# Performance work log

Measured on AMD Instinct MI355X. Metric: run time of the kernel, lower is better.

Reference implementation:

```python
import jax, jax.numpy as jnp
import numpy as np

NUM_HEADS = 16

def setup_inputs() -> dict:
    key = jax.random.key(0)
    ks = jax.random.split(key, 7)
    B, Q, K, D = 4, 512, 4096, 1024
    return {
        'query':  jax.random.normal(ks[0], (B, Q, D), dtype=jnp.float32),
        'memory': jax.random.normal(ks[1], (B, K, D), dtype=jnp.float32),
        'bias':   jax.random.normal(ks[2], (B, K), dtype=jnp.float32),
        'Wq': jax.random.normal(ks[3], (D, D), dtype=jnp.float32) * (D ** -0.5),
        'Wk': jax.random.normal(ks[4], (D, D), dtype=jnp.float32) * (D ** -0.5),
        'Wv': jax.random.normal(ks[5], (D, D), dtype=jnp.float32) * (D ** -0.5),
        'Wo': jax.random.normal(ks[6], (D, D), dtype=jnp.float32) * (D ** -0.5),
    }

def reference(query, memory, bias, Wq, Wk, Wv, Wo):
    B, Qn, _ = query.shape
    _, Kn, _ = memory.shape
    H = NUM_HEADS
    E = Wq.shape[1]
    dh = E // H
    scale = dh ** -0.5
    # projections (bias-free linears), split heads: [B, H, len, dh]
    q = (query @ Wq).reshape(B, Qn, H, dh).transpose(0, 2, 1, 3)
    k = (memory @ Wk).reshape(B, Kn, H, dh).transpose(0, 2, 1, 3)
    v = (memory @ Wv).reshape(B, Kn, H, dh).transpose(0, 2, 1, 3)
    scores = jnp.einsum('bhqd,bhkd->bhqk', q, k) * scale
    scores = scores + bias[:, None, None, :]          # additive support bias over K
    weights = jax.nn.softmax(scores, axis=-1)          # dropout p=0.0 -> identity
    out = jnp.einsum('bhqk,bhkd->bhqd', weights, v)
    out = out.transpose(0, 2, 1, 3).reshape(B, Qn, E)
    return out @ Wo
```

## Files before the change

kernel.cpp:

```cpp
#include <hip/hip_runtime.h>

typedef __attribute__((ext_vector_type(8))) short bf16x8;
typedef __attribute__((ext_vector_type(4))) short bf16x4;
typedef __attribute__((ext_vector_type(4))) float f32x4;

#define MFMA32(a,b,c) __builtin_amdgcn_mfma_f32_16x16x32_bf16((a),(b),(c),0,0,0)
#define MFMA16(a,b,c) __builtin_amdgcn_mfma_f32_16x16x16bf16_1k((a),(b),(c),0,0,0)
#define LOG2E 1.44269504f

__device__ __forceinline__ unsigned short f2bf(float f) {
  unsigned int u = __float_as_uint(f);
  u += 0x7fffu + ((u >> 16) & 1u);
  return (unsigned short)(u >> 16);
}

__device__ __forceinline__ void cp16(const void* g, void* l) {
  __builtin_amdgcn_global_load_lds((const __attribute__((address_space(1))) void*)g,
                                   (__attribute__((address_space(3))) void*)l, 16, 0, 0);
}

__global__ void conv_both(const float* __restrict__ q, const float* __restrict__ m,
                          const float* __restrict__ bias,
                          unsigned short* __restrict__ qo, unsigned short* __restrict__ mo,
                          float* __restrict__ bz) {
  int i = blockIdx.x * 256 + threadIdx.x;
  if (i < 524288) {
    float4 v = ((const float4*)q)[i];
    ushort4 o; o.x = f2bf(v.x); o.y = f2bf(v.y); o.z = f2bf(v.z); o.w = f2bf(v.w);
    ((ushort4*)qo)[i] = o;
  } else if (i < 4718592) {
    int j = i - 524288;
    float4 v = ((const float4*)m)[j];
    ushort4 o; o.x = f2bf(v.x); o.y = f2bf(v.y); o.z = f2bf(v.z); o.w = f2bf(v.w);
    ((ushort4*)mo)[j] = o;
  } else {
    int j = i - 4718592;
    float4 v = ((const float4*)bias)[j];
    float4 o;
    o.x = __builtin_fmaf(v.x, LOG2E, -16.f);
    o.y = __builtin_fmaf(v.y, LOG2E, -16.f);
    o.z = __builtin_fmaf(v.z, LOG2E, -16.f);
    o.w = __builtin_fmaf(v.w, LOG2E, -16.f);
    ((float4*)bz)[j] = o;
  }
}

__global__ void transpose4(const float* __restrict__ Wq, const float* __restrict__ Wk,
                           const float* __restrict__ Wv, const float* __restrict__ Wo,
                           unsigned short* __restrict__ dst) {
  __shared__ float t[32][33];
  int z = blockIdx.z;
  const float* W = (z == 0) ? Wq : (z == 1) ? Wk : (z == 2) ? Wv : Wo;
  unsigned short* WT = dst + (size_t)z * 1048576;
  int bx = blockIdx.x * 32, by = blockIdx.y * 32;
  int x = threadIdx.x, y0 = threadIdx.y;
#pragma unroll
  for (int r = 0; r < 4; ++r)
    t[y0 + r * 8][x] = W[(size_t)(by + y0 + r * 8) * 1024 + bx + x];
  __syncthreads();
#pragma unroll
  for (int r = 0; r < 4; ++r)
    WT[(size_t)(bx + y0 + r * 8) * 1024 + by + x] = f2bf(t[x][y0 + r * 8]);
}

__global__ __launch_bounds__(256, 2) void gemm_kv(
    const unsigned short* __restrict__ A,
    const unsigned short* __restrict__ Bk,
    const unsigned short* __restrict__ Bv,
    unsigned short* __restrict__ Kp,
    unsigned short* __restrict__ Vt)
{
  __shared__ __attribute__((aligned(16))) unsigned short lds[32768];
  const int tid = threadIdx.x;
  const int w = tid >> 6, lane = tid & 63;
  const int lh = lane & 15, q4 = lane >> 4;
  const int id = blockIdx.x;
  const int xcd = id & 7, j = id >> 3;
  const int tm = (xcd * 16 + (j >> 4)) * 128;
  const int tn = (j & 15) * 64;
  const int wm = (w >> 1) * 64, wn = (w & 1) * 32;

  const int r8 = lane >> 3;
  const int scol = ((lane & 7) ^ r8) * 8;
  const int srow = w * 8 + r8;
  const int fs0 = ((0 + q4) ^ (lh & 7)) * 8;
  const int fs1 = ((4 + q4) ^ (lh & 7)) * 8;

  const unsigned short* Ag = A  + (size_t)tm * 1024 + scol;
  const unsigned short* Kg = Bk + (size_t)tn * 1024 + scol;
  const unsigned short* Vg = Bv + (size_t)tn * 1024 + scol;

#define STG(BUF,KT) do {                                                      \
    cp16(Ag + (size_t)( 0 + srow) * 1024 + (KT)*64, lds + (BUF)*16384 +         w*512); \
    cp16(Ag + (size_t)(32 + srow) * 1024 + (KT)*64, lds + (BUF)*16384 +  2048 + w*512); \
    cp16(Ag + (size_t)(64 + srow) * 1024 + (KT)*64, lds + (BUF)*16384 +  4096 + w*512); \
    cp16(Ag + (size_t)(96 + srow) * 1024 + (KT)*64, lds + (BUF)*16384 +  6144 + w*512); \
    cp16(Kg + (size_t)( 0 + srow) * 1024 + (KT)*64, lds + (BUF)*16384 +  8192 + w*512); \
    cp16(Kg + (size_t)(32 + srow) * 1024 + (KT)*64, lds + (BUF)*16384 + 10240 + w*512); \
    cp16(Vg + (size_t)( 0 + srow) * 1024 + (KT)*64, lds + (BUF)*16384 + 12288 + w*512); \
    cp16(Vg + (size_t)(32 + srow) * 1024 + (KT)*64, lds + (BUF)*16384 + 14336 + w*512); \
  } while (0)

  f32x4 acck[4][2] = {}, accv[4][2] = {};

  STG(0, 0);

  for (int t = 0; t < 16; ++t) {
    const unsigned short* bse = lds + (t & 1) * 16384;
    __syncthreads();
    if (t < 15) STG((t & 1) ^ 1, t + 1);
    {
      bf16x8 a0[4], bk0[2], bv0[2];
#pragma unroll
      for (int m = 0; m < 4; ++m)
        a0[m] = *(const bf16x8*)(bse + (wm + m * 16 + lh) * 64 + fs0);
#pragma unroll
      for (int n = 0; n < 2; ++n) {
        bk0[n] = *(const bf16x8*)(bse +  8192 + (wn + n * 16 + lh) * 64 + fs0);
        bv0[n] = *(const bf16x8*)(bse + 12288 + (wn + n * 16 + lh) * 64 + fs0);
      }
      __builtin_amdgcn_s_setprio(1);
#pragma unroll
      for (int m = 0; m < 4; ++m)
#pragma unroll
        for (int n = 0; n < 2; ++n) {
          acck[m][n] = MFMA32(a0[m], bk0[n], acck[m][n]);
          accv[m][n] = MFMA32(a0[m], bv0[n], accv[m][n]);
        }
      __builtin_amdgcn_s_setprio(0);
    }
    {
      bf16x8 a1[4], bk1[2], bv1[2];
#pragma unroll
      for (int m = 0; m < 4; ++m)
        a1[m] = *(const bf16x8*)(bse + (wm + m * 16 + lh) * 64 + fs1);
#pragma unroll
      for (int n = 0; n < 2; ++n) {
        bk1[n] = *(const bf16x8*)(bse +  8192 + (wn + n * 16 + lh) * 64 + fs1);
        bv1[n] = *(const bf16x8*)(bse + 12288 + (wn + n * 16 + lh) * 64 + fs1);
      }
      __builtin_amdgcn_s_setprio(1);
#pragma unroll
      for (int m = 0; m < 4; ++m)
#pragma unroll
        for (int n = 0; n < 2; ++n) {
          acck[m][n] = MFMA32(a1[m], bk1[n], acck[m][n]);
          accv[m][n] = MFMA32(a1[m], bv1[n], accv[m][n]);
        }
      __builtin_amdgcn_s_setprio(0);
    }
  }
#undef STG

#pragma unroll
  for (int m = 0; m < 4; ++m)
#pragma unroll
    for (int n = 0; n < 2; ++n) {
      int row = tm + wm + m * 16 + q4 * 4;
      int col = tn + wn + n * 16 + lh;
#pragma unroll
      for (int e = 0; e < 4; ++e)
        Kp[(size_t)(row + e) * 1024 + col] = f2bf(acck[m][n][e]);
    }

  __syncthreads();
#pragma unroll
  for (int m = 0; m < 4; ++m)
#pragma unroll
    for (int n = 0; n < 2; ++n) {
      int row = wm + m * 16 + q4 * 4;
      int col = wn + n * 16 + lh;
      ushort4 v4;
      v4.x = f2bf(accv[m][n][0]); v4.y = f2bf(accv[m][n][1]);
      v4.z = f2bf(accv[m][n][2]); v4.w = f2bf(accv[m][n][3]);
      *(ushort4*)(lds + col * 128 + (row ^ ((col & 15) << 3))) = v4;
    }
  __syncthreads();
#pragma unroll
  for (int p = 0; p < 4; ++p) {
    int col = p * 16 + (tid >> 4);
    int jb = tid & 15;
    const unsigned short* src = lds + col * 128 + ((jb ^ (col & 15)) << 3);
    *(int4*)(Vt + (size_t)(tn + col) * 16384 + tm + jb * 8) = *(const int4*)src;
  }
}

__global__ __launch_bounds__(256) void gemm_bt64(
    const unsigned short* __restrict__ A, const unsigned short* __restrict__ B,
    float* __restrict__ Cf, unsigned short* __restrict__ Cb,
    int M, int N, int K, float scale)
{
  __shared__ __attribute__((aligned(16))) unsigned short lds[24576];
  int w = threadIdx.x >> 6, lane = threadIdx.x & 63;
  int lh = lane & 15, q4 = lane >> 4;
  int tm = blockIdx.y * 128, tn = blockIdx.x * 64;
  int wm = (w & 1) * 64, wn = (w >> 1) * 32;

  int srow = lane >> 2;
  int scol = ((lane & 3) ^ ((lane >> 3) & 3)) << 3;
  int q4s = (q4 ^ ((lh >> 1) & 3)) << 3;

#define STG64(BUF,K0)                                                          \
  {                                                                            \
    _Pragma("unroll") for (int i = 0; i < 2; ++i) {                            \
      int c = w * 2 + i;                                                       \
      cp16(A + (size_t)(tm + c * 16 + srow) * K + (K0) + scol,                 \
           lds + (BUF) * 6144 + c * 512);                                      \
    }                                                                          \
    cp16(B + (size_t)(tn + w * 16 + srow) * K + (K0) + scol,                   \
         lds + (BUF) * 6144 + 4096 + w * 512);                                 \
  }

  f32x4 acc[4][2] = {};
  const int nw = K >> 6;

  STG64(0, 0);
  STG64(1, 32);

  for (int s = 0; s < nw; ++s) {
    __syncthreads();
    if (s + 1 < nw) {
      STG64((2 * s + 2) & 3, (2 * s + 2) << 5);
      STG64((2 * s + 3) & 3, (2 * s + 3) << 5);
    }
#pragma unroll
    for (int u = 0; u < 2; ++u) {
      const unsigned short* bse = lds + ((2 * s + u) & 3) * 6144;
      bf16x8 afr[4], bfr[2];
#pragma unroll
      for (int r = 0; r < 4; ++r)
        afr[r] = *(const bf16x8*)(bse + (wm + r * 16 + lh) * 32 + q4s);
#pragma unroll
      for (int c = 0; c < 2; ++c)
        bfr[c] = *(const bf16x8*)(bse + 4096 + (wn + c * 16 + lh) * 32 + q4s);
      __builtin_amdgcn_s_setprio(1);
#pragma unroll
      for (int r = 0; r < 4; ++r)
#pragma unroll
        for (int c = 0; c < 2; ++c)
          acc[r][c] = MFMA32(afr[r], bfr[c], acc[r][c]);
      __builtin_amdgcn_s_setprio(0);
    }
  }
#undef STG64

#pragma unroll
  for (int r = 0; r < 4; ++r)
#pragma unroll
    for (int c = 0; c < 2; ++c)
#pragma unroll
      for (int e = 0; e < 4; ++e) {
        int row = tm + wm + r * 16 + q4 * 4 + e;
        int col = tn + wn + c * 16 + lh;
        if (Cb) Cb[(size_t)row * N + col] = f2bf(acc[r][c][e] * scale);
        else    Cf[(size_t)row * N + col] = acc[r][c][e] * scale;
      }
}

__global__ __launch_bounds__(256) void attn_kernel(
    const unsigned short* __restrict__ Q, const unsigned short* __restrict__ Kp,
    const unsigned short* __restrict__ VT, const float* __restrict__ bz,
    float* __restrict__ po, float* __restrict__ lp)
{
  __shared__ __attribute__((aligned(16))) unsigned short Klds[8192];
  __shared__ __attribute__((aligned(16))) unsigned short Vlds[8192];
  int w = threadIdx.x >> 6, lane = threadIdx.x & 63;
  int lh = lane & 15, q4 = lane >> 4;

  int id = blockIdx.x;
  int xcd = id & 7, j = id >> 3;
  int ql = j & 7;
  int half = ql & 1, qt = ql >> 1;
  int bh = (j >> 3) * 8 + xcd;
  int b = bh >> 4, h = bh & 15;
  int q0 = qt * 128;
  int t00 = half * 2048;

  const unsigned short* Qb = Q + (size_t)(b * 512 + q0 + w * 32) * 1024 + h * 64;
  const unsigned short* Kb = Kp + (size_t)(b * 4096) * 1024 + h * 64;
  const unsigned short* Vb = VT + (size_t)(h * 64) * 16384 + b * 4096;
  const float* bzg = bz + (size_t)b * 4096;

  bf16x8 bq[2][2];
#pragma unroll
  for (int s = 0; s < 2; ++s)
#pragma unroll
    for (int th = 0; th < 2; ++th)
      bq[s][th] = *(const bf16x8*)(Qb + (size_t)(s * 16 + lh) * 1024 + th * 32 + q4 * 8);

  f32x4 oa[2][4] = {};
  float ls[2] = {0.f, 0.f};

  int rl = lane >> 3, blk = lane & 7;
  int sw = ((blk ^ rl) * 8);

  {
    int t = t00;
#pragma unroll
    for (int r = 0; r < 2; ++r) {
      int seg = r * 4 + w;
      int row = seg * 8 + rl;
      cp16(Kb + (size_t)(t + row) * 1024 + sw, Klds + seg * 512);
      cp16(Vb + (size_t)row * 16384 + t + sw, Vlds + seg * 512);
    }
  }

  for (int ti = 0; ti < 32; ++ti) {
    int t = t00 + ti * 64;
    __syncthreads();
    if (ti < 31) {
      int t2 = t + 64;
      int bo2 = ((ti + 1) & 1) * 4096;
#pragma unroll
      for (int r = 0; r < 2; ++r) {
        int seg = r * 4 + w;
        int row = seg * 8 + rl;
        cp16(Kb + (size_t)(t2 + row) * 1024 + sw, Klds + bo2 + seg * 512);
        cp16(Vb + (size_t)row * 16384 + t2 + sw, Vlds + bo2 + seg * 512);
      }
    }
    const unsigned short* Kl = Klds + (ti & 1) * 4096;
    const unsigned short* Vl = Vlds + (ti & 1) * 4096;

    float4 bz4[4];
#pragma unroll
    for (int c = 0; c < 4; ++c)
      bz4[c] = *(const float4*)(bzg + t + c * 16 + q4 * 4);

    bf16x8 kf[4][2];
#pragma unroll
    for (int c = 0; c < 4; ++c)
#pragma unroll
      for (int th = 0; th < 2; ++th)
        kf[c][th] = *(const bf16x8*)(Kl + (c * 16 + lh) * 64 + (((th << 2) + q4) ^ (lh & 7)) * 8);
    bf16x4 vf[4][4];
#pragma unroll
    for (int c = 0; c < 4; ++c)
#pragma unroll
      for (int c2 = 0; c2 < 4; ++c2)
        vf[c][c2] = *(const bf16x4*)(Vl + (c2 * 16 + lh) * 64 +
                                     (((c << 1) + (q4 >> 1)) ^ (lh & 7)) * 8 + (q4 & 1) * 4);

#pragma unroll
    for (int s = 0; s < 2; ++s) {
#pragma unroll
      for (int c = 0; c < 4; ++c) {
        f32x4 z = {};
        z = MFMA32(kf[c][0], bq[s][0], z);
        z = MFMA32(kf[c][1], bq[s][1], z);
        float bzf[4] = {bz4[c].x, bz4[c].y, bz4[c].z, bz4[c].w};
        bf16x4 pb;
        float ps = 0.f;
#pragma unroll
        for (int e = 0; e < 4; ++e) {
          float p = __builtin_amdgcn_exp2f(z[e] + bzf[e]);
          ps += p;
          pb[e] = (short)f2bf(p);
        }
        ls[s] += ps;
#pragma unroll
        for (int c2 = 0; c2 < 4; ++c2)
          oa[s][c2] = MFMA16(vf[c][c2], pb, oa[s][c2]);
      }
    }
  }

#pragma unroll
  for (int s = 0; s < 2; ++s) {
    ls[s] += __shfl_xor(ls[s], 16);
    ls[s] += __shfl_xor(ls[s], 32);
  }

  int sl = bh * 4 + qt;
  float* pslice = po + (size_t)(half * 256 + sl) * 8192;
#pragma unroll
  for (int s = 0; s < 2; ++s) {
    if (q4 == 0) lp[half * 32768 + sl * 128 + w * 32 + s * 16 + lh] = ls[s];
#pragma unroll
    for (int c2 = 0; c2 < 4; ++c2)
#pragma unroll
      for (int e = 0; e < 4; ++e)
        pslice[(c2 * 16 + q4 * 4 + e) * 128 + w * 32 + s * 16 + lh] = oa[s][c2][e];
  }
}

__global__ void norm_kernel(const float* __restrict__ po, const float* __restrict__ lp,
                            unsigned short* __restrict__ ao) {
  int g = blockIdx.x * 256 + threadIdx.x;
  int d8 = (g & 7) * 8;
  int rowid = g >> 3;
  int bh = rowid >> 9, rq = rowid & 511, qt = rq >> 7, qcol = rq & 127;
  int sl = bh * 4 + qt;
  const float* p0 = po + (size_t)sl * 8192;
  const float* p1 = po + (size_t)(256 + sl) * 8192;
  float l = lp[sl * 128 + qcol] + lp[32768 + sl * 128 + qcol];
  float inv = 1.f / l;
  unsigned short o8[8];
#pragma unroll
  for (int k = 0; k < 8; ++k)
    o8[k] = f2bf((p0[(d8 + k) * 128 + qcol] + p1[(d8 + k) * 128 + qcol]) * inv);
  int b = bh >> 4, h = bh & 15;
  unsigned short* dst = ao + (size_t)(b * 512 + qt * 128 + qcol) * 1024 + h * 64 + d8;
  *(ushort4*)dst = *(ushort4*)o8;
  *(ushort4*)(dst + 4) = *(ushort4*)(o8 + 4);
}

extern "C" void kernel_launch(void* const* d_in, const int* in_sizes, int n_in,
                              void* d_out, int out_size, void* d_ws, size_t ws_size,
                              hipStream_t stream) {
  const float* query  = (const float*)d_in[0];
  const float* memory = (const float*)d_in[1];
  const float* bias   = (const float*)d_in[2];
  const float* Wq     = (const float*)d_in[3];
  const float* Wk     = (const float*)d_in[4];
  const float* Wv     = (const float*)d_in[5];
  const float* Wo     = (const float*)d_in[6];
  float* out = (float*)d_out;

  unsigned short* ws  = (unsigned short*)d_ws;
  unsigned short* qbf = ws;
  unsigned short* mbf = qbf + 2097152;
  unsigned short* WqT = mbf + 16777216;
  unsigned short* WkT = WqT + 1048576;
  unsigned short* WvT = WkT + 1048576;
  unsigned short* WoT = WvT + 1048576;
  unsigned short* qp  = WoT + 1048576;
  unsigned short* kp  = qp + 2097152;
  unsigned short* vT  = kp + 16777216;
  unsigned short* ao  = vT + 16777216;
  float* bzw = (float*)(ao + 2097152);
  float* po = (float*)ws;
  float* lp = po + 4194304;

  conv_both<<<18448, 256, 0, stream>>>(query, memory, bias, qbf, mbf, bzw);
  transpose4<<<dim3(32, 32, 4), dim3(32, 8), 0, stream>>>(Wq, Wk, Wv, Wo, WqT);

  gemm_bt64<<<dim3(16, 16), 256, 0, stream>>>(qbf, WqT, nullptr, qp, 2048, 1024, 1024, 0.125f * LOG2E);
  gemm_kv<<<2048, 256, 0, stream>>>(mbf, WkT, WvT, kp, vT);

  attn_kernel<<<512, 256, 0, stream>>>(qp, kp, vT, bzw, po, lp);
  norm_kernel<<<1024, 256, 0, stream>>>(po, lp, ao);

  gemm_bt64<<<dim3(16, 16), 256, 0, stream>>>(ao, WoT, out, nullptr, 2048, 1024, 1024, 1.f);
}
```

Measured before the change: 290.5 us.

## Rewrite K/V projection GEMM as 256x256 tiles with an 8-wave pipelined schedule

The combined K/V projection kernel now treats WkT and WvT as one contiguous 2048-row B matrix and computes 256x256 output tiles with 512-thread blocks. Previously each block did a 128x64 tile for each of K and V. Global-to-LDS staging is split into fine-grained phases interleaved with MFMA work, using explicit vmcnt waits and raw barriers. The goal is more data reuse per LDS load, fewer blocks, and better overlap of loads with compute. In exchange it uses 128KB of LDS, more accumulator registers, and hand-tuned wait counts that must match the issue order exactly.

```diff
diff --git a/kernel.cpp b/kernel.cpp
--- a/kernel.cpp
+++ b/kernel.cpp
@@ -7,6 +7,9 @@
 #define MFMA32(a,b,c) __builtin_amdgcn_mfma_f32_16x16x32_bf16((a),(b),(c),0,0,0)
 #define MFMA16(a,b,c) __builtin_amdgcn_mfma_f32_16x16x16bf16_1k((a),(b),(c),0,0,0)
 #define LOG2E 1.44269504f
+
+#define VMW_(n) asm volatile("s_waitcnt vmcnt(" #n ")" ::: "memory")
+#define VMW(n) VMW_(n)
 
 __device__ __forceinline__ unsigned short f2bf(float f) {
   unsigned int u = __float_as_uint(f);
@@ -63,125 +66,125 @@
     WT[(size_t)(bx + y0 + r * 8) * 1024 + by + x] = f2bf(t[x][y0 + r * 8]);
 }
 
-__global__ __launch_bounds__(256, 2) void gemm_kv(
+__global__ __launch_bounds__(512, 2) void gemm_kv(
     const unsigned short* __restrict__ A,
-    const unsigned short* __restrict__ Bk,
-    const unsigned short* __restrict__ Bv,
+    const unsigned short* __restrict__ B,
     unsigned short* __restrict__ Kp,
     unsigned short* __restrict__ Vt)
 {
-  __shared__ __attribute__((aligned(16))) unsigned short lds[32768];
+  __shared__ __attribute__((aligned(16))) unsigned short lds[65536];
   const int tid = threadIdx.x;
   const int w = tid >> 6, lane = tid & 63;
   const int lh = lane & 15, q4 = lane >> 4;
   const int id = blockIdx.x;
   const int xcd = id & 7, j = id >> 3;
-  const int tm = (xcd * 16 + (j >> 4)) * 128;
-  const int tn = (j & 15) * 64;
-  const int wm = (w >> 1) * 64, wn = (w & 1) * 32;
-
-  const int r8 = lane >> 3;
-  const int scol = ((lane & 7) ^ r8) * 8;
-  const int srow = w * 8 + r8;
+  const int tm = (xcd * 8 + (j >> 3)) * 256;
+  const int tn = (j & 7) * 256;
+  const int wm = (w >> 2) * 128;
+  const int bn = (w & 3) * 64;
+
   const int fs0 = ((0 + q4) ^ (lh & 7)) * 8;
   const int fs1 = ((4 + q4) ^ (lh & 7)) * 8;
-
-  const unsigned short* Ag = A  + (size_t)tm * 1024 + scol;
-  const unsigned short* Kg = Bk + (size_t)tn * 1024 + scol;
-  const unsigned short* Vg = Bv + (size_t)tn * 1024 + scol;
-
-#define STG(BUF,KT) do {                                                      \
-    cp16(Ag + (size_t)( 0 + srow) * 1024 + (KT)*64, lds + (BUF)*16384 +         w*512); \
-    cp16(Ag + (size_t)(32 + srow) * 1024 + (KT)*64, lds + (BUF)*16384 +  2048 + w*512); \
-    cp16(Ag + (size_t)(64 + srow) * 1024 + (KT)*64, lds + (BUF)*16384 +  4096 + w*512); \
-    cp16(Ag + (size_t)(96 + srow) * 1024 + (KT)*64, lds + (BUF)*16384 +  6144 + w*512); \
-    cp16(Kg + (size_t)( 0 + srow) * 1024 + (KT)*64, lds + (BUF)*16384 +  8192 + w*512); \
-    cp16(Kg + (size_t)(32 + srow) * 1024 + (KT)*64, lds + (BUF)*16384 + 10240 + w*512); \
-    cp16(Vg + (size_t)( 0 + srow) * 1024 + (KT)*64, lds + (BUF)*16384 + 12288 + w*512); \
-    cp16(Vg + (size_t)(32 + srow) * 1024 + (KT)*64, lds + (BUF)*16384 + 14336 + w*512); \
+  const int a_off = (wm >> 7) * 4096 + lh * 64;
+  const int ub = (w >> 1) & 1;
+  const int b_off = 32768 + ub * 8192 + ((bn & 64) + lh) * 64;
+
+  const int r0 = w * 16 + (lane >> 3), r1 = r0 + 8;
+  const int scol = ((lane & 7) ^ ((lane >> 3) & 7)) * 8;
+  const int am0 = (r0 >> 6) * 128 + (r0 & 63);
+  const int am1 = (r1 >> 6) * 128 + (r1 & 63);
+  const unsigned short* Ag = A + (size_t)tm * 1024 + scol;
+  const unsigned short* Bg = B + (size_t)tn * 1024 + scol;
+  const int dstc = w * 1024;
+
+#define STG_A(T,U) do { \
+    cp16(Ag + (size_t)(am0 + (U)*64) * 1024 + (T)*64, lds + (((T)&1)*16384) + (U)*8192 + dstc); \
+    cp16(Ag + (size_t)(am1 + (U)*64) * 1024 + (T)*64, lds + (((T)&1)*16384) + (U)*8192 + dstc + 512); \
   } while (0)
-
-  f32x4 acck[4][2] = {}, accv[4][2] = {};
-
-  STG(0, 0);
-
-  for (int t = 0; t < 16; ++t) {
-    const unsigned short* bse = lds + (t & 1) * 16384;
+#define STG_B(T,U) do { \
+    cp16(Bg + (size_t)((U)*128 + r0) * 1024 + (T)*64, lds + 32768 + (((T)&1)*16384) + (U)*8192 + dstc); \
+    cp16(Bg + (size_t)((U)*128 + r1) * 1024 + (T)*64, lds + 32768 + (((T)&1)*16384) + (U)*8192 + dstc + 512); \
+  } while (0)
+
+  f32x4 acc[8][4] = {};
+  bf16x8 afr[4], bfr[4];
+
+#define PHASE(PAR, MH, FS, BL, WC, SC) do {                                   \
+    WC;                                                                       \
+    asm volatile("s_waitcnt lgkmcnt(0)" ::: "memory");                        \
+    asm volatile("s_barrier" ::: "memory");                                   \
+    if (BL) {                                                                 \
+      _Pragma("unroll") for (int nf = 0; nf < 4; ++nf)                        \
+        bfr[nf] = *(const bf16x8*)(lds + b_off + (PAR)*16384 + nf*1024 + (FS)); \
+    }                                                                         \
+    _Pragma("unroll") for (int mf = 0; mf < 4; ++mf)                          \
+      afr[mf] = *(const bf16x8*)(lds + a_off + (PAR)*16384 + (MH)*8192 + mf*1024 + (FS)); \
+    SC;                                                                       \
+    __builtin_amdgcn_s_setprio(1);                                            \
+    _Pragma("unroll") for (int mf = 0; mf < 4; ++mf)                          \
+      _Pragma("unroll") for (int nf = 0; nf < 4; ++nf)                        \
+        acc[(MH)*4+mf][nf] = MFMA32(afr[mf], bfr[nf], acc[(MH)*4+mf][nf]);    \
+    __builtin_amdgcn_s_setprio(0);                                            \
+  } while (0)
+
+  STG_B(0, 0); STG_B(0, 1); STG_A(0, 0); STG_A(0, 1); STG_A(1, 0);
+
+  for (int i = 0; i < 7; ++i) {
+    const int T = 2 * i;
+    PHASE(0, 0, fs0, 1, VMW(4),  STG_A(T + 1, 1));
+    PHASE(0, 1, fs0, 0, VMW(4),  STG_B(T + 1, 0));
+    PHASE(0, 0, fs1, 1, (void)0, STG_B(T + 1, 1));
+    PHASE(0, 1, fs1, 0, (void)0, STG_B(T + 2, 0));
+    PHASE(1, 0, fs0, 1, VMW(2),  STG_B(T + 2, 1));
+    PHASE(1, 1, fs0, 0, (void)0, STG_A(T + 2, 0));
+    PHASE(1, 0, fs1, 1, (void)0, STG_A(T + 2, 1));
+    PHASE(1, 1, fs1, 0, (void)0, STG_A(T + 3, 0));
+  }
+  PHASE(0, 0, fs0, 1, VMW(4),  STG_A(15, 1));
+  PHASE(0, 1, fs0, 0, VMW(4),  STG_B(15, 0));
+  PHASE(0, 0, fs1, 1, (void)0, STG_B(15, 1));
+  PHASE(0, 1, fs1, 0, (void)0, (void)0);
+  PHASE(1, 0, fs0, 1, VMW(0),  (void)0);
+  PHASE(1, 1, fs0, 0, (void)0, (void)0);
+  PHASE(1, 0, fs1, 1, (void)0, (void)0);
+  PHASE(1, 1, fs1, 0, (void)0, (void)0);
+
+#undef PHASE
+#undef STG_A
+#undef STG_B
+
+  if (tn < 1024) {
+#pragma unroll
+    for (int am = 0; am < 8; ++am)
+#pragma unroll
+      for (int nf = 0; nf < 4; ++nf) {
+        int row = tm + wm + (am >> 2) * 64 + (am & 3) * 16 + q4 * 4;
+        int col = tn + bn + nf * 16 + lh;
+#pragma unroll
+        for (int e = 0; e < 4; ++e)
+          Kp[(size_t)(row + e) * 1024 + col] = f2bf(acc[am][nf][e]);
+      }
+  } else {
     __syncthreads();
-    if (t < 15) STG((t & 1) ^ 1, t + 1);
-    {
-      bf16x8 a0[4], bk0[2], bv0[2];
-#pragma unroll
-      for (int m = 0; m < 4; ++m)
-        a0[m] = *(const bf16x8*)(bse + (wm + m * 16 + lh) * 64 + fs0);
-#pragma unroll
-      for (int n = 0; n < 2; ++n) {
-        bk0[n] = *(const bf16x8*)(bse +  8192 + (wn + n * 16 + lh) * 64 + fs0);
-        bv0[n] = *(const bf16x8*)(bse + 12288 + (wn + n * 16 + lh) * 64 + fs0);
+#pragma unroll
+    for (int am = 0; am < 8; ++am)
+#pragma unroll
+      for (int nf = 0; nf < 4; ++nf) {
+        int lrow = wm + (am >> 2) * 64 + (am & 3) * 16 + q4 * 4;
+        int lcol = bn + nf * 16 + lh;
+        ushort4 v4;
+        v4.x = f2bf(acc[am][nf][0]); v4.y = f2bf(acc[am][nf][1]);
+        v4.z = f2bf(acc[am][nf][2]); v4.w = f2bf(acc[am][nf][3]);
+        *(ushort4*)(lds + lcol * 256 + (lrow ^ ((lcol & 31) << 3))) = v4;
       }
-      __builtin_amdgcn_s_setprio(1);
-#pragma unroll
-      for (int m = 0; m < 4; ++m)
-#pragma unroll
-        for (int n = 0; n < 2; ++n) {
-          acck[m][n] = MFMA32(a0[m], bk0[n], acck[m][n]);
-          accv[m][n] = MFMA32(a0[m], bv0[n], accv[m][n]);
-        }
-      __builtin_amdgcn_s_setprio(0);
-    }
-    {
-      bf16x8 a1[4], bk1[2], bv1[2];
-#pragma unroll
-      for (int m = 0; m < 4; ++m)
-        a1[m] = *(const bf16x8*)(bse + (wm + m * 16 + lh) * 64 + fs1);
-#pragma unroll
-      for (int n = 0; n < 2; ++n) {
-        bk1[n] = *(const bf16x8*)(bse +  8192 + (wn + n * 16 + lh) * 64 + fs1);
-        bv1[n] = *(const bf16x8*)(bse + 12288 + (wn + n * 16 + lh) * 64 + fs1);
-      }
-      __builtin_amdgcn_s_setprio(1);
-#pragma unroll
-      for (int m = 0; m < 4; ++m)
-#pragma unroll
-        for (int n = 0; n < 2; ++n) {
-          acck[m][n] = MFMA32(a1[m], bk1[n], acck[m][n]);
-          accv[m][n] = MFMA32(a1[m], bv1[n], accv[m][n]);
-        }
-      __builtin_amdgcn_s_setprio(0);
-    }
-  }
-#undef STG
-
-#pragma unroll
-  for (int m = 0; m < 4; ++m)
-#pragma unroll
-    for (int n = 0; n < 2; ++n) {
-      int row = tm + wm + m * 16 + q4 * 4;
-      int col = tn + wn + n * 16 + lh;
-#pragma unroll
-      for (int e = 0; e < 4; ++e)
-        Kp[(size_t)(row + e) * 1024 + col] = f2bf(acck[m][n][e]);
-    }
-
-  __syncthreads();
-#pragma unroll
-  for (int m = 0; m < 4; ++m)
-#pragma unroll
-    for (int n = 0; n < 2; ++n) {
-      int row = wm + m * 16 + q4 * 4;
-      int col = wn + n * 16 + lh;
-      ushort4 v4;
-      v4.x = f2bf(accv[m][n][0]); v4.y = f2bf(accv[m][n][1]);
-      v4.z = f2bf(accv[m][n][2]); v4.w = f2bf(accv[m][n][3]);
-      *(ushort4*)(lds + col * 128 + (row ^ ((col & 15) << 3))) = v4;
-    }
-  __syncthreads();
-#pragma unroll
-  for (int p = 0; p < 4; ++p) {
-    int col = p * 16 + (tid >> 4);
-    int jb = tid & 15;
-    const unsigned short* src = lds + col * 128 + ((jb ^ (col & 15)) << 3);
-    *(int4*)(Vt + (size_t)(tn + col) * 16384 + tm + jb * 8) = *(const int4*)src;
+    __syncthreads();
+#pragma unroll
+    for (int p = 0; p < 16; ++p) {
+      int colg = p * 16 + (tid >> 5);
+      int jb = tid & 31;
+      const unsigned short* src = lds + colg * 256 + ((jb ^ (colg & 31)) << 3);
+      *(int4*)(Vt + (size_t)(tn - 1024 + colg) * 16384 + tm + jb * 8) = *(const int4*)src;
+    }
   }
 }
 
@@ -436,7 +439,7 @@
   transpose4<<<dim3(32, 32, 4), dim3(32, 8), 0, stream>>>(Wq, Wk, Wv, Wo, WqT);
 
   gemm_bt64<<<dim3(16, 16), 256, 0, stream>>>(qbf, WqT, nullptr, qp, 2048, 1024, 1024, 0.125f * LOG2E);
-  gemm_kv<<<2048, 256, 0, stream>>>(mbf, WkT, WvT, kp, vT);
+  gemm_kv<<<512, 512, 0, stream>>>(mbf, WkT, kp, vT);
 
   attn_kernel<<<512, 256, 0, stream>>>(qp, kp, vT, bzw, po, lp);
   norm_kernel<<<1024, 256, 0, stream>>>(po, lp, ao);
```

After: 292.0 us. About the same (+0.5%).
